# Performance work log

Hardware: AMD Instinct MI355X
Metric: run time of the kernel (lower is better)

Reference implementation:

```python
import jax, jax.numpy as jnp
import numpy as np

HIDDEN = 2048
N_HEADS = 16
N_KV = 4
HEAD_DIM = 128
SEQ = 2048
BATCH = 2
THETA = 10000.0


def rotate_half(x):
    half = x.shape[-1] // 2
    x1, x2 = x[..., :half], x[..., half:]
    return jnp.concatenate((-x2, x1), axis=-1)


def rope_cos_sin(seq_len, dim, theta, dtype):
    inv_freq = 1.0 / (theta ** (jnp.arange(0, dim, 2, dtype=jnp.float32) / dim))
    t = jnp.arange(seq_len, dtype=jnp.float32)
    freqs = jnp.einsum('i,j->ij', t, inv_freq)            # [S, dim/2]
    emb = jnp.concatenate((freqs, freqs), axis=-1)        # [S, dim]
    return jnp.cos(emb).astype(dtype), jnp.sin(emb).astype(dtype)


def setup_inputs() -> dict:
    key = jax.random.key(0)
    kx, kq, kk, kv, ko = jax.random.split(key, 5)
    s = 0.02
    return {
        'x':  jax.random.normal(kx, (BATCH, SEQ, HIDDEN), dtype=jnp.float32),
        'Wq': jax.random.normal(kq, (HIDDEN, N_HEADS * HEAD_DIM), dtype=jnp.float32) * s,
        'Wk': jax.random.normal(kk, (HIDDEN, N_KV * HEAD_DIM), dtype=jnp.float32) * s,
        'Wv': jax.random.normal(kv, (HIDDEN, N_KV * HEAD_DIM), dtype=jnp.float32) * s,
        'Wo': jax.random.normal(ko, (N_HEADS * HEAD_DIM, HIDDEN), dtype=jnp.float32) * s,
    }


def reference(x, Wq, Wk, Wv, Wo):
    B, S, _ = x.shape
    q = (x @ Wq).reshape(B, S, N_HEADS, HEAD_DIM)
    k = (x @ Wk).reshape(B, S, N_KV, HEAD_DIM)
    v = (x @ Wv).reshape(B, S, N_KV, HEAD_DIM)

    cos, sin = rope_cos_sin(S, HEAD_DIM, THETA, x.dtype)
    cos = cos[None, :, None, :]  # [1,S,1,D]
    sin = sin[None, :, None, :]
    q = q * cos + rotate_half(q) * sin
    k = k * cos + rotate_half(k) * sin

    repeat = N_HEADS // N_KV
    k = jnp.repeat(k, repeat, axis=2)  # repeat_interleave over heads
    v = jnp.repeat(v, repeat, axis=2)

    # [B,H,S,D]
    q = q.transpose(0, 2, 1, 3)
    k = k.transpose(0, 2, 1, 3)
    v = v.transpose(0, 2, 1, 3)

    scale = HEAD_DIM ** -0.5
    scores = jnp.einsum('bhqd,bhkd->bhqk', q, k) * scale
    causal = jnp.triu(jnp.full((S, S), -jnp.inf, dtype=scores.dtype), k=1)
    scores = scores + causal
    probs = jax.nn.softmax(scores, axis=-1)
    out = jnp.einsum('bhqk,bhkd->bhqd', probs, v)
    out = out.transpose(0, 2, 1, 3).reshape(B, S, N_HEADS * HEAD_DIM)
    return out @ Wo
```

## Files before the change

### kernel.cpp

```cpp
#include <hip/hip_runtime.h>
#include <hip/hip_bf16.h>
#include <math.h>

#define HIDDEN 2048
#define NHEADS 16
#define NKV 4
#define HD 128
#define SEQ 2048
#define BATCH 2
#define MTOT (BATCH*SEQ)
#define NQ (NHEADS*HD)
#define NKVD (NKV*HD)
#define NQKV (NQ + 2*NKVD)

typedef __attribute__((ext_vector_type(8))) short short8;
typedef __attribute__((ext_vector_type(4))) float float4v;

#if __has_builtin(__builtin_amdgcn_exp2f)
#define EXP2F __builtin_amdgcn_exp2f
#else
#define EXP2F exp2f
#endif
#define C1 0.1275174f

static __device__ __forceinline__ unsigned short f2bf(float f) {
  union { float f; unsigned int u; } v; v.f = f;
  unsigned int r = v.u + 0x7FFF + ((v.u >> 16) & 1);
  return (unsigned short)(r >> 16);
}
static __device__ __forceinline__ float bf2f(unsigned short h) {
  union { unsigned int u; float f; } v; v.u = ((unsigned int)h) << 16;
  return v.f;
}

static __device__ __forceinline__ void async16(const unsigned short* g, unsigned short* l) {
  __builtin_amdgcn_global_load_lds(
      (const __attribute__((address_space(1))) unsigned int*)g,
      (__attribute__((address_space(3))) unsigned int*)l, 16, 0, 0);
}

__global__ void prep(const float* __restrict__ x, unsigned short* __restrict__ xb,
                     const float* __restrict__ Wq, const float* __restrict__ Wk,
                     const float* __restrict__ Wv, const float* __restrict__ Wo,
                     unsigned short* __restrict__ Wqt, unsigned short* __restrict__ Wkt,
                     unsigned short* __restrict__ Wvt, unsigned short* __restrict__ Wot) {
  __shared__ float tile[32][33];
  int bx = blockIdx.x;
  if (bx < 8192) {
    int i = (bx * 256 + threadIdx.x) * 4;
    float4 v = *(const float4*)(x + i);
    ushort4 o;
    o.x = f2bf(v.x); o.y = f2bf(v.y); o.z = f2bf(v.z); o.w = f2bf(v.w);
    *(ushort4*)(xb + i) = o;
    return;
  }
  int bz = bx - 8192;
  int tbx = bz % 160, tby = bz / 160;
  const int K = 2048;
  const float* W; unsigned short* Wt; int N; int tn;
  if (tbx < 64)      { W = Wq; Wt = Wqt; N = NQ;     tn = tbx * 32; }
  else if (tbx < 80) { W = Wk; Wt = Wkt; N = NKVD;   tn = (tbx - 64) * 32; }
  else if (tbx < 96) { W = Wv; Wt = Wvt; N = NKVD;   tn = (tbx - 80) * 32; }
  else               { W = Wo; Wt = Wot; N = HIDDEN; tn = (tbx - 96) * 32; }
  int tk = tby * 32;
  int tx = threadIdx.x & 31;
  int ty = threadIdx.x >> 5;
  #pragma unroll
  for (int i = 0; i < 4; i++) {
    int k = tk + ty + i * 8;
    tile[ty + i * 8][tx] = W[(size_t)k * N + tn + tx];
  }
  __syncthreads();
  #pragma unroll
  for (int i = 0; i < 4; i++) {
    int n = tn + ty + i * 8;
    Wt[(size_t)n * K + tk + tx] = f2bf(tile[tx][ty + i * 8]);
  }
}

__global__ void rope_all(unsigned short* __restrict__ Qb,
                         unsigned short* __restrict__ Kb) {
  int idx = blockIdx.x * blockDim.x + threadIdx.x;
  const int QTOT = MTOT * NHEADS * 64;
  unsigned short* P; int nheads;
  if (idx < QTOT) { P = Qb; nheads = NHEADS; }
  else            { P = Kb; nheads = NKV; idx -= QTOT; }
  int d = idx & 63;
  int hr = idx >> 6;
  int spos = (hr / nheads) % SEQ;
  size_t base = (size_t)hr * HD;
  float inv = exp2f((float)d * -0.2076205059304601f);
  float ang = (float)spos * inv;
  float sn, cs;
  sincosf(ang, &sn, &cs);
  float q1 = bf2f(P[base + d]);
  float q2 = bf2f(P[base + d + 64]);
  P[base + d]      = f2bf(q1 * cs - q2 * sn);
  P[base + d + 64] = f2bf(q2 * cs + q1 * sn);
}

__global__ __launch_bounds__(1024, 4) void gemm_qkv(
    const unsigned short* __restrict__ A,
    const unsigned short* __restrict__ Bt,
    unsigned short* __restrict__ Qb,
    unsigned short* __restrict__ Kb,
    unsigned short* __restrict__ Vt) {
  __shared__ __align__(16) unsigned short L[4 * 16384];
  const int K = HIDDEN;
  const int NT = K / 32;
  int bm = blockIdx.y * 256, bn = blockIdx.x * 256;
  int tid = threadIdx.x, w = tid >> 6, lane = tid & 63;
  int wrow = w >> 2, wcol = w & 3;
  int m16 = lane & 15, quad = lane >> 4;
  int r = tid >> 2, lch = tid & 3;
  int lchs = lch ^ ((r >> 1) & 3);
  int qx = quad ^ ((m16 >> 1) & 3);
  const unsigned short* Agp = A + (size_t)(bm + r) * K + lchs * 8;
  const unsigned short* Bgp = Bt + (size_t)(bn + r) * K + lchs * 8;

  float4v acc[4][4];
  #pragma unroll
  for (int i = 0; i < 4; i++)
    #pragma unroll
    for (int j = 0; j < 4; j++) acc[i][j] = (float4v)0.0f;

  auto stage = [&](int t) {
    unsigned short* Lb = L + (t & 3) * 16384;
    int k0 = t * 32;
    async16(Agp + k0, Lb + tid * 8);
    async16(Bgp + k0, Lb + 8192 + tid * 8);
  };

  const bool isV = (blockIdx.x >= 10);

  stage(0); stage(1);
  asm volatile("s_waitcnt vmcnt(2)" ::: "memory");
  __builtin_amdgcn_s_barrier();
  __builtin_amdgcn_sched_barrier(0);

  if (!isV) {
    for (int t = 0; t < NT; ++t) {
      if (t + 2 < NT) stage(t + 2);
      const unsigned short* Ab_ = L + (t & 3) * 16384;
      const unsigned short* Bb_ = Ab_ + 8192;
      short8 af[4], bfr[4];
      #pragma unroll
      for (int i = 0; i < 4; i++)
        af[i] = *(const short8*)(&Ab_[(wrow * 64 + i * 16 + m16) * 32 + qx * 8]);
      #pragma unroll
      for (int j = 0; j < 4; j++)
        bfr[j] = *(const short8*)(&Bb_[(wcol * 64 + j * 16 + m16) * 32 + qx * 8]);
      __builtin_amdgcn_s_setprio(1);
      #pragma unroll
      for (int i = 0; i < 4; i++)
        #pragma unroll
        for (int j = 0; j < 4; j++)
          acc[i][j] = __builtin_amdgcn_mfma_f32_16x16x32_bf16(af[i], bfr[j], acc[i][j], 0, 0, 0);
      __builtin_amdgcn_s_setprio(0);
      if (t + 2 < NT) { asm volatile("s_waitcnt vmcnt(2)" ::: "memory"); }
      else            { asm volatile("s_waitcnt vmcnt(0)" ::: "memory"); }
      __builtin_amdgcn_s_barrier();
      __builtin_amdgcn_sched_barrier(0);
    }
  } else {
    for (int t = 0; t < NT; ++t) {
      if (t + 2 < NT) stage(t + 2);
      const unsigned short* Ab_ = L + (t & 3) * 16384;
      const unsigned short* Bb_ = Ab_ + 8192;
      short8 af[4], bfr[4];
      #pragma unroll
      for (int i = 0; i < 4; i++)
        af[i] = *(const short8*)(&Ab_[(wrow * 64 + i * 16 + m16) * 32 + qx * 8]);
      #pragma unroll
      for (int j = 0; j < 4; j++)
        bfr[j] = *(const short8*)(&Bb_[(wcol * 64 + j * 16 + m16) * 32 + qx * 8]);
      __builtin_amdgcn_s_setprio(1);
      #pragma unroll
      for (int i = 0; i < 4; i++)
        #pragma unroll
        for (int j = 0; j < 4; j++)
          acc[i][j] = __builtin_amdgcn_mfma_f32_16x16x32_bf16(bfr[j], af[i], acc[i][j], 0, 0, 0);
      __builtin_amdgcn_s_setprio(0);
      if (t + 2 < NT) { asm volatile("s_waitcnt vmcnt(2)" ::: "memory"); }
      else            { asm volatile("s_waitcnt vmcnt(0)" ::: "memory"); }
      __builtin_amdgcn_s_barrier();
      __builtin_amdgcn_sched_barrier(0);
    }
  }

  if (blockIdx.x < 8) {
    #pragma unroll
    for (int i = 0; i < 4; i++)
      #pragma unroll
      for (int j = 0; j < 4; j++)
        #pragma unroll
        for (int rr = 0; rr < 4; rr++) {
          int row = bm + wrow * 64 + i * 16 + quad * 4 + rr;
          int col = bn + wcol * 64 + j * 16 + m16;
          Qb[(size_t)row * NQ + col] = f2bf(acc[i][j][rr]);
        }
  } else if (!isV) {
    #pragma unroll
    for (int i = 0; i < 4; i++)
      #pragma unroll
      for (int j = 0; j < 4; j++)
        #pragma unroll
        for (int rr = 0; rr < 4; rr++) {
          int row = bm + wrow * 64 + i * 16 + quad * 4 + rr;
          int col = bn - 2048 + wcol * 64 + j * 16 + m16;
          Kb[(size_t)row * NKVD + col] = f2bf(acc[i][j][rr]);
        }
  } else {
    #pragma unroll
    for (int i = 0; i < 4; i++)
      #pragma unroll
      for (int j = 0; j < 4; j++)
        #pragma unroll
        for (int rr = 0; rr < 4; rr++) {
          int f = bn - 2560 + wcol * 64 + j * 16 + quad * 4 + rr;
          int m = bm + wrow * 64 + i * 16 + m16;
          Vt[(size_t)f * MTOT + m] = f2bf(acc[i][j][rr]);
        }
  }
}

__global__ __launch_bounds__(512, 4) void gemm_o(
    const unsigned short* __restrict__ A,
    const unsigned short* __restrict__ Bt,
    float* __restrict__ C, int M, int N, int K) {
  __shared__ __align__(16) unsigned short L[4 * 8192];
  const int NT = K / 32;
  int bm = blockIdx.y * 128, bn = blockIdx.x * 128;
  int tid = threadIdx.x, w = tid >> 6, lane = tid & 63;
  int wrow = w >> 2, wcol = w & 3;
  int m16 = lane & 15, quad = lane >> 4;
  int r = tid >> 2, lch = tid & 3;
  int lchs = lch ^ ((r >> 1) & 3);
  int qx = quad ^ ((m16 >> 1) & 3);
  const unsigned short* Agp = A + (size_t)(bm + r) * K + lchs * 8;
  const unsigned short* Bgp = Bt + (size_t)(bn + r) * K + lchs * 8;

  float4v acc[4][2];
  #pragma unroll
  for (int i = 0; i < 4; i++)
    #pragma unroll
    for (int j = 0; j < 2; j++) acc[i][j] = (float4v)0.0f;

  auto stage = [&](int t) {
    unsigned short* Lb = L + (t & 3) * 8192;
    int k0 = t * 32;
    async16(Agp + k0, Lb + tid * 8);
    async16(Bgp + k0, Lb + 4096 + tid * 8);
  };

  stage(0); stage(1);
  asm volatile("s_waitcnt vmcnt(2)" ::: "memory");
  __builtin_amdgcn_s_barrier();
  __builtin_amdgcn_sched_barrier(0);

  for (int t = 0; t < NT; ++t) {
    if (t + 2 < NT) stage(t + 2);
    const unsigned short* Ab_ = L + (t & 3) * 8192;
    const unsigned short* Bb_ = Ab_ + 4096;
    short8 af[4], bfr[2];
    #pragma unroll
    for (int i = 0; i < 4; i++)
      af[i] = *(const short8*)(&Ab_[(wrow * 64 + i * 16 + m16) * 32 + qx * 8]);
    #pragma unroll
    for (int j = 0; j < 2; j++)
      bfr[j] = *(const short8*)(&Bb_[(wcol * 32 + j * 16 + m16) * 32 + qx * 8]);
    __builtin_amdgcn_s_setprio(1);
    #pragma unroll
    for (int i = 0; i < 4; i++)
      #pragma unroll
      for (int j = 0; j < 2; j++)
        acc[i][j] = __builtin_amdgcn_mfma_f32_16x16x32_bf16(af[i], bfr[j], acc[i][j], 0, 0, 0);
    __builtin_amdgcn_s_setprio(0);
    if (t + 2 < NT) { asm volatile("s_waitcnt vmcnt(2)" ::: "memory"); }
    else            { asm volatile("s_waitcnt vmcnt(0)" ::: "memory"); }
    __builtin_amdgcn_s_barrier();
    __builtin_amdgcn_sched_barrier(0);
  }

  #pragma unroll
  for (int i = 0; i < 4; i++)
    #pragma unroll
    for (int j = 0; j < 2; j++)
      #pragma unroll
      for (int rr = 0; rr < 4; rr++) {
        int row = bm + wrow * 64 + i * 16 + quad * 4 + rr;
        int col = bn + wcol * 32 + j * 16 + m16;
        C[(size_t)row * N + col] = acc[i][j][rr];
      }
}

#define FLASH_TILE(CUR, NXT)                                                  \
  {                                                                           \
    const int ktb = kt * 64;                                                  \
    __syncthreads();        \
    {                                                                         \
      const unsigned short* Vg = Vt + vgrow * (size_t)MTOT                    \
                                    + (size_t)b * SEQ + ktb + kcv * 32 + vlch * 8; \
      unsigned short* Vl = Vs + kcv * 4096 + ipv * 512;                       \
      _Pragma("unroll")                                                       \
      for (int i = 0; i < 4; i++) async16(Vg + (size_t)i * 16 * MTOT, Vl + i * 512); \
    }                                                                         \
    if (kt < H) {                                                             \
      const unsigned short* Kg = Kp + (((size_t)b * SEQ + (kt + 1) * 64 + lrow) * NKV + kvh) * HD + w * 32 + vlch * 8; \
      unsigned short* Kl = NXT + w * 2048;                                    \
      _Pragma("unroll")                                                       \
      for (int i = 0; i < 4; i++) async16(Kg + (size_t)i * 16 * NKV * HD, Kl + i * 512); \
    }                                                                         \
    const bool act1 = (ktb <= lmax_w);                                        \
    float4v sacc[2][4];                                                       \
    _Pragma("unroll") for (int s4 = 0; s4 < 4; s4++) {                        \
      sacc[0][s4] = (float4v)0.0f; sacc[1][s4] = (float4v)0.0f; }             \
    __builtin_amdgcn_s_setprio(1);                                            \
    if (act1) {                                                               \
      _Pragma("unroll")                                                       \
      for (int s4 = 0; s4 < 4; s4++)                                          \
        _Pragma("unroll")                                                     \
        for (int c = 0; c < 4; c++) {                                         \
          short8 kf = *(const short8*)(&CUR[c * 2048 + (s4 * 16 + m16) * 32 + qx * 8]); \
          sacc[0][s4] = __builtin_amdgcn_mfma_f32_16x16x32_bf16(kf, qf[0][c], sacc[0][s4], 0, 0, 0); \
          sacc[1][s4] = __builtin_amdgcn_mfma_f32_16x16x32_bf16(kf, qf[1][c], sacc[1][s4], 0, 0, 0); \
        }                                                                     \
    } else {                                                                  \
      _Pragma("unroll")                                                       \
      for (int s4 = 0; s4 < 4; s4++)                                          \
        _Pragma("unroll")                                                     \
        for (int c = 0; c < 4; c++) {                                         \
          short8 kf = *(const short8*)(&CUR[c * 2048 + (s4 * 16 + m16) * 32 + qx * 8]); \
          sacc[0][s4] = __builtin_amdgcn_mfma_f32_16x16x32_bf16(kf, qf[0][c], sacc[0][s4], 0, 0, 0); \
        }                                                                     \
    }                                                                         \
    __builtin_amdgcn_s_setprio(0);                                            \
    _Pragma("unroll")                                                         \
    for (int qs = 0; qs < 2; qs++) {                                          \
      if (qs == 0 || act1) {                                                  \
        const int tb = qs ? L : H;                                            \
        const int qabs = tb * 64 + w * 16 + m16;                              \
        const bool diag = (kt == tb);                                         \
        float sv[4][4]; float mloc = -1e30f;                                  \
        if (diag) {                                                           \
          _Pragma("unroll") for (int s4 = 0; s4 < 4; s4++)                    \
            _Pragma("unroll") for (int rr = 0; rr < 4; rr++) {                \
              int kabs = ktb + s4 * 16 + quad * 4 + rr;                       \
              float t = sacc[qs][s4][rr];                                     \
              sv[s4][rr] = (kabs > qabs) ? -1e30f : t;                        \
              mloc = fmaxf(mloc, sv[s4][rr]); }                               \
        } else {                                                              \
          _Pragma("unroll") for (int s4 = 0; s4 < 4; s4++)                    \
            _Pragma("unroll") for (int rr = 0; rr < 4; rr++) {                \
              sv[s4][rr] = sacc[qs][s4][rr]; mloc = fmaxf(mloc, sv[s4][rr]); } \
        }                                                                     \
        mloc *= C1;                                                           \
        mloc = fmaxf(mloc, __shfl_xor(mloc, 16, 64));                         \
        mloc = fmaxf(mloc, __shfl_xor(mloc, 32, 64));                         \
        float mnewS = fmaxf(miS[qs], mloc);                                   \
        const bool defer = (bool)__all(mloc <= miS[qs] + 8.0f);               \
        if (defer) mnewS = miS[qs];  \
        const int prow = qs * 64 + w * 16 + m16;                              \
        const int psw = prow * 32; const int rx = prow & 7;                   \
        float rs = 0.0f;                                                      \
        _Pragma("unroll") for (int s4 = 0; s4 < 4; s4++) {                    \
          float p0 = EXP2F(__builtin_fmaf(sv[s4][0], C1, -mnewS));            \
          float p1 = EXP2F(__builtin_fmaf(sv[s4][1], C1, -mnewS));            \
          float p2 = EXP2F(__builtin_fmaf(sv[s4][2], C1, -mnewS));            \
          float p3 = EXP2F(__builtin_fmaf(sv[s4][3], C1, -mnewS));            \
          rs += p0 + p1 + p2 + p3;                                            \
          uint2 u;                                                            \
          u.x = (__float_as_uint(p1) & 0xffff0000u) | (__float_as_uint(p0) >> 16); \
          u.y = (__float_as_uint(p3) & 0xffff0000u) | (__float_as_uint(p2) >> 16); \
          int chunkW = s4 * 2 + (quad >> 1);                                  \
          *(uint2*)(&Ps[psw + ((chunkW ^ rx) << 2) + (quad & 1) * 2]) = u;    \
        }                                                                     \
        rs += __shfl_xor(rs, 16, 64);                                         \
        rs += __shfl_xor(rs, 32, 64);                                         \
        if (!defer) {                                                         \
          const float alpha = EXP2F(miS[qs] - mnewS);                         \
          li[qs] *= alpha; miS[qs] = mnewS;                                   \
          _Pragma("unroll") for (int ds = 0; ds < 8; ds++) oacc[ds][qs] *= alpha; \
        }                                                                     \
        li[qs] += rs;                                                         \
      }                                                                       \
    }                                                                         \
    __syncthreads();     \
    {                                                                         \
      const int r0 = w * 16 + m16, r1 = 64 + w * 16 + m16;                    \
      __builtin_amdgcn_s_setprio(1);                                          \
      if (act1) {                                                             \
        _Pragma("unroll")                                                     \
        for (int kc = 0; kc < 2; kc++) {                                      \
          short8 pf0 = *(const short8*)(&Ps[r0 * 32 + (((kc * 4 + quad) ^ (r0 & 7)) << 2)]); \
          short8 pf1 = *(const short8*)(&Ps[r1 * 32 + (((kc * 4 + quad) ^ (r1 & 7)) << 2)]); \
          _Pragma("unroll")                                                   \
          for (int ds = 0; ds < 8; ds++) {                                    \
            short8 vf = *(const short8*)(&Vs[kc * 4096 + (ds * 16 + m16) * 32 + qx * 8]); \
            oacc[ds][0] = __builtin_amdgcn_mfma_f32_16x16x32_bf16(vf, pf0, oacc[ds][0], 0, 0, 0); \
            oacc[ds][1] = __builtin_amdgcn_mfma_f32_16x16x32_bf16(vf, pf1, oacc[ds][1], 0, 0, 0); \
          }                                                                   \
        }                                                                     \
      } else {                                                                \
        _Pragma("unroll")                                                     \
        for (int kc = 0; kc < 2; kc++) {                                      \
          short8 pf0 = *(const short8*)(&Ps[r0 * 32 + (((kc * 4 + quad) ^ (r0 & 7)) << 2)]); \
          _Pragma("unroll")                                                   \
          for (int ds = 0; ds < 8; ds++) {                                    \
            short8 vf = *(const short8*)(&Vs[kc * 4096 + (ds * 16 + m16) * 32 + qx * 8]); \
            oacc[ds][0] = __builtin_amdgcn_mfma_f32_16x16x32_bf16(vf, pf0, oacc[ds][0], 0, 0, 0); \
          }                                                                   \
        }                                                                     \
      }                                                                       \
      __builtin_amdgcn_s_setprio(0);                                          \
    }                                                                         \
  }

__global__ __launch_bounds__(256, 2) void flash_attn(
    const unsigned short* __restrict__ Q,
    const unsigned short* __restrict__ Kp,
    const unsigned short* __restrict__ Vt,
    unsigned short* __restrict__ O) {
  __shared__ unsigned short Ks0[4 * 64 * 32];
  __shared__ unsigned short Ks1[4 * 64 * 32];
  __shared__ unsigned short Vs[2 * 128 * 32];
  __shared__ unsigned int   Ps[128 * 32];

  int bx = blockIdx.x;
  int h  = blockIdx.y;
  int b  = blockIdx.z;
  int kvh = h >> 2;
  int H = 31 - bx, L = bx;
  int tid = threadIdx.x;
  int w = tid >> 6, lane = tid & 63;
  int m16 = lane & 15, quad = lane >> 4;
  int lrow = lane >> 2, lch = lane & 3;
  const int vlch = lch ^ ((lrow >> 1) & 3);
  const int qx = quad ^ ((m16 >> 1) & 3);
  const int lmax_w = L * 64 + w * 16 + 15;

  const int kcv = w >> 1, ipv = (w & 1) * 4;
  const size_t vgrow = (size_t)kvh * HD + ipv * 16 + lrow;

  short8 qf[2][4];
  #pragma unroll
  for (int qs = 0; qs < 2; qs++) {
    int tb = qs ? L : H;
    size_t qbase = (((size_t)b * SEQ + tb * 64 + w * 16 + m16) * NHEADS + h) * HD;
    #pragma unroll
    for (int c = 0; c < 4; c++)
      qf[qs][c] = *(const short8*)(Q + qbase + c * 32 + quad * 8);
  }

  float4v oacc[8][2];
  #pragma unroll
  for (int ds = 0; ds < 8; ds++) { oacc[ds][0] = (float4v)0.0f; oacc[ds][1] = (float4v)0.0f; }
  float miS[2] = {-1e30f, -1e30f}, li[2] = {0.0f, 0.0f};

  {
    const unsigned short* Kg = Kp + (((size_t)b * SEQ + lrow) * NKV + kvh) * HD + w * 32 + vlch * 8;
    unsigned short* Kl = Ks0 + w * 2048;
    #pragma unroll
    for (int i = 0; i < 4; i++) async16(Kg + (size_t)i * 16 * NKV * HD, Kl + i * 512);
  }

  int kt = 0;
  for (;;) {
    FLASH_TILE(Ks0, Ks1)
    if (++kt > H) break;
    FLASH_TILE(Ks1, Ks0)
    if (++kt > H) break;
  }

  #pragma unroll
  for (int qs = 0; qs < 2; qs++) {
    float inv = 1.0f / li[qs];
    int tb = qs ? L : H;
    int qabs = tb * 64 + w * 16 + m16;
    size_t obase = (((size_t)b * SEQ + qabs) * NHEADS + h) * HD + quad * 4;
    #pragma unroll
    for (int ds = 0; ds < 8; ds++) {
      float v0 = oacc[ds][qs][0] * inv;
      float v1 = oacc[ds][qs][1] * inv;
      float v2 = oacc[ds][qs][2] * inv;
      float v3 = oacc[ds][qs][3] * inv;
      uint2 u;
      u.x = ((unsigned)f2bf(v1) << 16) | f2bf(v0);
      u.y = ((unsigned)f2bf(v3) << 16) | f2bf(v2);
      *(uint2*)(O + obase + ds * 16) = u;
    }
  }
}

extern "C" void kernel_launch(void* const* d_in, const int* in_sizes, int n_in,
                              void* d_out, int out_size, void* d_ws, size_t ws_size,
                              hipStream_t stream) {
  const float* x  = (const float*)d_in[0];
  const float* Wq = (const float*)d_in[1];
  const float* Wk = (const float*)d_in[2];
  const float* Wv = (const float*)d_in[3];
  const float* Wo = (const float*)d_in[4];
  float* out = (float*)d_out;

  unsigned short* ws = (unsigned short*)d_ws;
  unsigned short* xb  = ws;
  unsigned short* Wqt = xb  + (size_t)MTOT * HIDDEN;
  unsigned short* Wkt = Wqt + (size_t)NQ * HIDDEN;
  unsigned short* Wvt = Wkt + (size_t)NKVD * HIDDEN;
  unsigned short* Wot = Wvt + (size_t)NKVD * HIDDEN;
  unsigned short* Qb  = Wot + (size_t)NQ * HIDDEN;
  unsigned short* Kb  = Qb  + (size_t)MTOT * NQ;
  unsigned short* Vtb = Kb  + (size_t)MTOT * NKVD;
  unsigned short* Ab  = Vtb + (size_t)MTOT * NKVD;

  prep<<<8192 + 160 * 64, 256, 0, stream>>>(x, xb, Wq, Wk, Wv, Wo, Wqt, Wkt, Wvt, Wot);

  gemm_qkv<<<dim3(NQKV / 256, MTOT / 256), 1024, 0, stream>>>(xb, Wqt, Qb, Kb, Vtb);

  rope_all<<<(MTOT * (NHEADS + NKV) * 64) / 256, 256, 0, stream>>>(Qb, Kb);

  flash_attn<<<dim3(16, NHEADS, BATCH), 256, 0, stream>>>(Qb, Kb, Vtb, Ab);

  gemm_o<<<dim3(HIDDEN / 128, MTOT / 128), 512, 0, stream>>>(Ab, Wot, out, MTOT, HIDDEN, NQ);
}
```

Measured before the change: 291.7 us.

## Fuse RoPE into QKV GEMM epilogue by remapping warp tiles to full heads

```diff
diff --git a/kernel.cpp b/kernel.cpp
--- a/kernel.cpp
+++ b/kernel.cpp
@@ -78,27 +78,6 @@
   }
 }
 
-__global__ void rope_all(unsigned short* __restrict__ Qb,
-                         unsigned short* __restrict__ Kb) {
-  int idx = blockIdx.x * blockDim.x + threadIdx.x;
-  const int QTOT = MTOT * NHEADS * 64;
-  unsigned short* P; int nheads;
-  if (idx < QTOT) { P = Qb; nheads = NHEADS; }
-  else            { P = Kb; nheads = NKV; idx -= QTOT; }
-  int d = idx & 63;
-  int hr = idx >> 6;
-  int spos = (hr / nheads) % SEQ;
-  size_t base = (size_t)hr * HD;
-  float inv = exp2f((float)d * -0.2076205059304601f);
-  float ang = (float)spos * inv;
-  float sn, cs;
-  sincosf(ang, &sn, &cs);
-  float q1 = bf2f(P[base + d]);
-  float q2 = bf2f(P[base + d + 64]);
-  P[base + d]      = f2bf(q1 * cs - q2 * sn);
-  P[base + d + 64] = f2bf(q2 * cs + q1 * sn);
-}
-
 __global__ __launch_bounds__(1024, 4) void gemm_qkv(
     const unsigned short* __restrict__ A,
     const unsigned short* __restrict__ Bt,
@@ -110,7 +89,6 @@
   const int NT = K / 32;
   int bm = blockIdx.y * 256, bn = blockIdx.x * 256;
   int tid = threadIdx.x, w = tid >> 6, lane = tid & 63;
-  int wrow = w >> 2, wcol = w & 3;
   int m16 = lane & 15, quad = lane >> 4;
   int r = tid >> 2, lch = tid & 3;
   int lchs = lch ^ ((r >> 1) & 3);
@@ -118,12 +96,6 @@
   const unsigned short* Agp = A + (size_t)(bm + r) * K + lchs * 8;
   const unsigned short* Bgp = Bt + (size_t)(bn + r) * K + lchs * 8;
 
-  float4v acc[4][4];
-  #pragma unroll
-  for (int i = 0; i < 4; i++)
-    #pragma unroll
-    for (int j = 0; j < 4; j++) acc[i][j] = (float4v)0.0f;
-
   auto stage = [&](int t) {
     unsigned short* Lb = L + (t & 3) * 16384;
     int k0 = t * 32;
@@ -132,6 +104,7 @@
   };
 
   const bool isV = (blockIdx.x >= 10);
+  const bool isK = (blockIdx.x >= 8 && blockIdx.x < 10);
 
   stage(0); stage(1);
   asm volatile("s_waitcnt vmcnt(2)" ::: "memory");
@@ -139,22 +112,28 @@
   __builtin_amdgcn_sched_barrier(0);
 
   if (!isV) {
+    int wrow2 = w >> 1, wcol2 = w & 1;
+    float4v acc[2][8];
+    #pragma unroll
+    for (int i = 0; i < 2; i++)
+      #pragma unroll
+      for (int j = 0; j < 8; j++) acc[i][j] = (float4v)0.0f;
     for (int t = 0; t < NT; ++t) {
       if (t + 2 < NT) stage(t + 2);
       const unsigned short* Ab_ = L + (t & 3) * 16384;
       const unsigned short* Bb_ = Ab_ + 8192;
-      short8 af[4], bfr[4];
-      #pragma unroll
-      for (int i = 0; i < 4; i++)
-        af[i] = *(const short8*)(&Ab_[(wrow * 64 + i * 16 + m16) * 32 + qx * 8]);
-      #pragma unroll
-      for (int j = 0; j < 4; j++)
-        bfr[j] = *(const short8*)(&Bb_[(wcol * 64 + j * 16 + m16) * 32 + qx * 8]);
+      short8 af[2], bfr[8];
+      #pragma unroll
+      for (int i = 0; i < 2; i++)
+        af[i] = *(const short8*)(&Ab_[(wrow2 * 32 + i * 16 + m16) * 32 + qx * 8]);
+      #pragma unroll
+      for (int j = 0; j < 8; j++)
+        bfr[j] = *(const short8*)(&Bb_[(wcol2 * 128 + j * 16 + m16) * 32 + qx * 8]);
       __builtin_amdgcn_s_setprio(1);
       #pragma unroll
-      for (int i = 0; i < 4; i++)
+      for (int i = 0; i < 2; i++)
         #pragma unroll
-        for (int j = 0; j < 4; j++)
+        for (int j = 0; j < 8; j++)
           acc[i][j] = __builtin_amdgcn_mfma_f32_16x16x32_bf16(af[i], bfr[j], acc[i][j], 0, 0, 0);
       __builtin_amdgcn_s_setprio(0);
       if (t + 2 < NT) { asm volatile("s_waitcnt vmcnt(2)" ::: "memory"); }
@@ -162,7 +141,34 @@
       __builtin_amdgcn_s_barrier();
       __builtin_amdgcn_sched_barrier(0);
     }
+    unsigned short* Out = isK ? Kb : Qb;
+    const int ncols = isK ? NKVD : NQ;
+    const int cb = isK ? bn - 2048 : bn;
+    #pragma unroll
+    for (int i = 0; i < 2; i++)
+      #pragma unroll
+      for (int rr = 0; rr < 4; rr++) {
+        int row = bm + wrow2 * 32 + i * 16 + quad * 4 + rr;
+        float spos = (float)(row & (SEQ - 1));
+        #pragma unroll
+        for (int j = 0; j < 4; j++) {
+          int d = j * 16 + m16;
+          float inv = exp2f((float)d * -0.2076205059304601f);
+          float sn, cs;
+          sincosf(spos * inv, &sn, &cs);
+          float f1 = acc[i][j][rr], f2 = acc[i][j + 4][rr];
+          int col = cb + wcol2 * 128 + j * 16 + m16;
+          Out[(size_t)row * ncols + col]      = f2bf(f1 * cs - f2 * sn);
+          Out[(size_t)row * ncols + col + 64] = f2bf(f2 * cs + f1 * sn);
+        }
+      }
   } else {
+    int wrow = w >> 2, wcol = w & 3;
+    float4v acc[4][4];
+    #pragma unroll
+    for (int i = 0; i < 4; i++)
+      #pragma unroll
+      for (int j = 0; j < 4; j++) acc[i][j] = (float4v)0.0f;
     for (int t = 0; t < NT; ++t) {
       if (t + 2 < NT) stage(t + 2);
       const unsigned short* Ab_ = L + (t & 3) * 16384;
@@ -186,31 +192,6 @@
       __builtin_amdgcn_s_barrier();
       __builtin_amdgcn_sched_barrier(0);
     }
-  }
-
-  if (blockIdx.x < 8) {
-    #pragma unroll
-    for (int i = 0; i < 4; i++)
-      #pragma unroll
-      for (int j = 0; j < 4; j++)
-        #pragma unroll
-        for (int rr = 0; rr < 4; rr++) {
-          int row = bm + wrow * 64 + i * 16 + quad * 4 + rr;
-          int col = bn + wcol * 64 + j * 16 + m16;
-          Qb[(size_t)row * NQ + col] = f2bf(acc[i][j][rr]);
-        }
-  } else if (!isV) {
-    #pragma unroll
-    for (int i = 0; i < 4; i++)
-      #pragma unroll
-      for (int j = 0; j < 4; j++)
-        #pragma unroll
-        for (int rr = 0; rr < 4; rr++) {
-          int row = bm + wrow * 64 + i * 16 + quad * 4 + rr;
-          int col = bn - 2048 + wcol * 64 + j * 16 + m16;
-          Kb[(size_t)row * NKVD + col] = f2bf(acc[i][j][rr]);
-        }
-  } else {
     #pragma unroll
     for (int i = 0; i < 4; i++)
       #pragma unroll
@@ -517,8 +498,6 @@
 
   gemm_qkv<<<dim3(NQKV / 256, MTOT / 256), 1024, 0, stream>>>(xb, Wqt, Qb, Kb, Vtb);
 
-  rope_all<<<(MTOT * (NHEADS + NKV) * 64) / 256, 256, 0, stream>>>(Qb, Kb);
-
   flash_attn<<<dim3(16, NHEADS, BATCH), 256, 0, stream>>>(Qb, Kb, Vtb, Ab);
 
   gemm_o<<<dim3(HIDDEN / 128, MTOT / 128), 512, 0, stream>>>(Ab, Wot, out, MTOT, HIDDEN, NQ);
```

Result: faster. 277.3 us (-4.9%).
